# Kernel optimization log

Measured on AMD Instinct MI355X. Metric: run time of the kernel, lower is better.

## Reference

```python
import jax, jax.numpy as jnp
import numpy as np

N_LAYERS = 4   # last-4 BERT hidden layers summed by _Encoder
B, L, D = 4, 512, 768
LIN, ENT = 128, 10


def setup_inputs() -> dict:
    key = jax.random.key(0)
    k1, k2, k3, k4, k5 = jax.random.split(key, 5)
    return {
        "hidden_states": jax.random.normal(k1, (N_LAYERS, B, L, D), dtype=jnp.float32),
        "w_span": jax.random.normal(k2, (LIN, 2 * D), dtype=jnp.float32) * 0.02,
        "b_span": jax.random.normal(k3, (LIN,), dtype=jnp.float32) * 0.02,
        "w_cls": jax.random.normal(k4, (ENT, LIN), dtype=jnp.float32) * 0.02,
        "b_cls": jax.random.normal(k5, (ENT,), dtype=jnp.float32) * 0.02,
    }


def reference(hidden_states, w_span, b_span, w_cls, b_cls):
    # _Encoder: sum of last-4 hidden layers -> token embeddings (b, L, d)
    tok = jnp.sum(hidden_states, axis=0)
    d = tok.shape[-1]
    # Decompose span_linear weight into i-half and j-half so we never
    # materialize the (b, L, L, 2d) concat tensor. By linearity:
    #   Linear(cat(tok_i, tok_j)) = tok_i @ W1^T + tok_j @ W2^T + b
    w_i, w_j = w_span[:, :d], w_span[:, d:]
    proj_i = jnp.einsum("bld,od->blo", tok, w_i)   # (b, L, lin)
    proj_j = jnp.einsum("bld,od->blo", tok, w_j)   # (b, L, lin)
    span = proj_i[:, :, None, :] + proj_j[:, None, :, :] + b_span  # (b, L, L, lin)
    scores = jnp.einsum("bijo,co->bijc", span, w_cls) + b_cls      # (b, L, L, ent)
    return jnp.transpose(scores, (0, 3, 1, 2))  # (b, ent, L, L)
```

## Files before the change

### kernel.cpp

```cpp
#include <hip/hip_runtime.h>

#define NLAYER 4
#define BB 4
#define LL 512
#define DD 768
#define NLIN 128
#define NENT 10

#define OFF_CONST 15360
#define OFF_SI    15376
#define OFF_SJ    35856

__global__ void __launch_bounds__(256) fuse_weights(
    const float* __restrict__ w_span,
    const float* __restrict__ b_span,
    const float* __restrict__ w_cls,
    const float* __restrict__ b_cls,
    float* __restrict__ ws)
{
    int t = blockIdx.x * 256 + threadIdx.x;
    float* weff   = ws;
    float* constc = ws + OFF_CONST;

    if (t < 20 * DD) {
        int c2 = t / DD;
        int d  = t - c2 * DD;
        int ci   = (c2 < NENT) ? c2 : c2 - NENT;
        int half = (c2 < NENT) ? 0  : 1;
        const float* wc    = w_cls + ci * NLIN;
        const float* wsrow = w_span + half * DD + d;
        float acc = 0.f;
        #pragma unroll 8
        for (int o = 0; o < NLIN; ++o)
            acc += wc[o] * wsrow[(size_t)o * (2 * DD)];
        weff[c2 * DD + d] = acc;
    }
    if (t < NENT) {
        float cc = b_cls[t];
        const float* wc = w_cls + t * NLIN;
        for (int o = 0; o < NLIN; ++o) cc += b_span[o] * wc[o];
        constc[t] = cc;
    }
}

__global__ void __launch_bounds__(256) reduce_proj(
    const float* __restrict__ hs,
    const float* __restrict__ wsro,
    float* __restrict__ si,
    float* __restrict__ sj)
{
    __shared__ float wsh[20 * DD];

    {
        const float4* src = (const float4*)wsro;
        float4*       dst = (float4*)wsh;
        #pragma unroll
        for (int r = 0; r < 15; ++r)
            dst[r * 256 + threadIdx.x] = src[r * 256 + threadIdx.x];
    }
    __syncthreads();

    const int wave = (blockIdx.x * 256 + threadIdx.x) >> 6;
    const int lane = threadIdx.x & 63;
    const int b = wave >> 9;
    const int l = wave & 511;

    const size_t LAYER_STRIDE = (size_t)BB * LL * DD;
    const size_t base = (size_t)(b * LL + l) * DD;

    float acc[20];
    #pragma unroll
    for (int c = 0; c < 20; ++c) acc[c] = 0.f;

    #pragma unroll
    for (int k = 0; k < 3; ++k) {
        const int d0 = k * 256 + lane * 4;
        const float* hp = hs + base + d0;
        float4 t0 = *(const float4*)(hp);
        float4 t1 = *(const float4*)(hp + LAYER_STRIDE);
        float4 t2 = *(const float4*)(hp + 2 * LAYER_STRIDE);
        float4 t3 = *(const float4*)(hp + 3 * LAYER_STRIDE);
        float4 tv;
        tv.x = t0.x + t1.x + t2.x + t3.x;
        tv.y = t0.y + t1.y + t2.y + t3.y;
        tv.z = t0.z + t1.z + t2.z + t3.z;
        tv.w = t0.w + t1.w + t2.w + t3.w;
        const float* wbase = wsh + d0;
        #pragma unroll
        for (int c = 0; c < 20; ++c) {
            float4 w = *(const float4*)(wbase + c * DD);
            acc[c] += tv.x * w.x + tv.y * w.y + tv.z * w.z + tv.w * w.w;
        }
    }

    #pragma unroll
    for (int c = 0; c < 20; ++c) {
        float v = acc[c];
        v += __shfl_xor(v, 1,  64);
        v += __shfl_xor(v, 2,  64);
        v += __shfl_xor(v, 4,  64);
        v += __shfl_xor(v, 8,  64);
        v += __shfl_xor(v, 16, 64);
        v += __shfl_xor(v, 32, 64);
        acc[c] = v;
    }

    if (lane == 0) {
        const float* constc = wsro + OFF_CONST;
        const int rb = b * NENT;
        #pragma unroll
        for (int c = 0; c < NENT; ++c) {
            si[(rb + c) * LL + l] = acc[c] + constc[c];
            sj[(rb + c) * LL + l] = acc[10 + c];
        }
    }
}

__global__ void __launch_bounds__(256) fill_out(
    const float* __restrict__ si,
    const float* __restrict__ sj,
    float* __restrict__ out)
{
    const int idx4 = blockIdx.x * 256 + threadIdx.x;
    const int j4 = idx4 & 127;
    const int i  = (idx4 >> 7) & 511;
    const int bc = idx4 >> 16;
    const float  s  = si[bc * LL + i];
    const float4 v  = ((const float4*)(sj + bc * LL))[j4];
    float4 o;
    o.x = s + v.x; o.y = s + v.y; o.z = s + v.z; o.w = s + v.w;
    ((float4*)out)[idx4] = o;
}

extern "C" void kernel_launch(void* const* d_in, const int* in_sizes, int n_in,
                              void* d_out, int out_size, void* d_ws, size_t ws_size,
                              hipStream_t stream) {
    const float* hs     = (const float*)d_in[0];
    const float* w_span = (const float*)d_in[1];
    const float* b_span = (const float*)d_in[2];
    const float* w_cls  = (const float*)d_in[3];
    const float* b_cls  = (const float*)d_in[4];
    float* ws  = (float*)d_ws;
    float* out = (float*)d_out;
    float* si = ws + OFF_SI;
    float* sj = ws + OFF_SJ;

    fuse_weights<<<60, 256, 0, stream>>>(w_span, b_span, w_cls, b_cls, ws);
    reduce_proj<<<512, 256, 0, stream>>>(hs, ws, si, sj);
    fill_out<<<10240, 256, 0, stream>>>(si, sj, out);
}
```

Baseline: 105.1 us.

## Split weight fusion 4-way, prefetch hidden states before LDS staging, nontemporal output stores

fuse_weights now gives each output element to four threads, each covering a quarter of the 128-wide reduction, and combines them with shuffles, so the launch grows from 60 to 241 blocks. reduce_proj issues its hidden-state loads (nontemporal) into registers before writing the staged weights to shared memory, so global latency overlaps with the LDS fill and barrier. fill_out writes the large output with nontemporal stores to reduce cache pollution. The cost is higher register pressure in reduce_proj from holding 15 staged vectors plus 12 prefetched vectors.

Result: faster. 98.13 us (-6.7%).

```diff
diff --git a/kernel.cpp b/kernel.cpp
--- a/kernel.cpp
+++ b/kernel.cpp
@@ -11,6 +11,8 @@
 #define OFF_SI    15376
 #define OFF_SJ    35856
 
+typedef float vfloat4 __attribute__((ext_vector_type(4)));
+
 __global__ void __launch_bounds__(256) fuse_weights(
     const float* __restrict__ w_span,
     const float* __restrict__ b_span,
@@ -18,28 +20,36 @@
     const float* __restrict__ b_cls,
     float* __restrict__ ws)
 {
-    int t = blockIdx.x * 256 + threadIdx.x;
+    const int t   = blockIdx.x * 256 + threadIdx.x;
+    const int sub = t & 3;
+    const int idx = t >> 2;
     float* weff   = ws;
     float* constc = ws + OFF_CONST;
 
-    if (t < 20 * DD) {
-        int c2 = t / DD;
-        int d  = t - c2 * DD;
-        int ci   = (c2 < NENT) ? c2 : c2 - NENT;
-        int half = (c2 < NENT) ? 0  : 1;
-        const float* wc    = w_cls + ci * NLIN;
-        const float* wsrow = w_span + half * DD + d;
+    if (idx < 20 * DD) {
+        const int c2 = idx / DD;
+        const int d  = idx - c2 * DD;
+        const int ci   = (c2 < NENT) ? c2 : c2 - NENT;
+        const int half = (c2 < NENT) ? 0  : 1;
+        const float* wc    = w_cls + ci * NLIN + sub * 32;
+        const float* wsrow = w_span + (size_t)sub * 32 * (2 * DD) + half * DD + d;
         float acc = 0.f;
-        #pragma unroll 8
-        for (int o = 0; o < NLIN; ++o)
+        #pragma unroll
+        for (int o = 0; o < 32; ++o)
             acc += wc[o] * wsrow[(size_t)o * (2 * DD)];
-        weff[c2 * DD + d] = acc;
-    }
-    if (t < NENT) {
-        float cc = b_cls[t];
-        const float* wc = w_cls + t * NLIN;
-        for (int o = 0; o < NLIN; ++o) cc += b_span[o] * wc[o];
-        constc[t] = cc;
+        acc += __shfl_xor(acc, 1, 64);
+        acc += __shfl_xor(acc, 2, 64);
+        if (sub == 0) weff[c2 * DD + d] = acc;
+    } else if (idx < 20 * DD + NENT) {
+        const int c = idx - 20 * DD;
+        const float* wc = w_cls + c * NLIN + sub * 32;
+        const float* bs = b_span + sub * 32;
+        float cc = (sub == 0) ? b_cls[c] : 0.f;
+        #pragma unroll
+        for (int o = 0; o < 32; ++o) cc += bs[o] * wc[o];
+        cc += __shfl_xor(cc, 1, 64);
+        cc += __shfl_xor(cc, 2, 64);
+        if (sub == 0) constc[c] = cc;
     }
 }
 
@@ -51,22 +61,36 @@
 {
     __shared__ float wsh[20 * DD];
 
-    {
-        const float4* src = (const float4*)wsro;
-        float4*       dst = (float4*)wsh;
-        #pragma unroll
-        for (int r = 0; r < 15; ++r)
-            dst[r * 256 + threadIdx.x] = src[r * 256 + threadIdx.x];
-    }
-    __syncthreads();
-
-    const int wave = (blockIdx.x * 256 + threadIdx.x) >> 6;
-    const int lane = threadIdx.x & 63;
+    const int tid  = threadIdx.x;
+    const int wave = (blockIdx.x * 256 + tid) >> 6;
+    const int lane = tid & 63;
     const int b = wave >> 9;
     const int l = wave & 511;
 
     const size_t LAYER_STRIDE = (size_t)BB * LL * DD;
     const size_t base = (size_t)(b * LL + l) * DD;
+
+    const vfloat4* src = (const vfloat4*)wsro;
+    vfloat4 stg[15];
+    #pragma unroll
+    for (int r = 0; r < 15; ++r)
+        stg[r] = src[r * 256 + tid];
+
+    vfloat4 t0[3], t1[3], t2[3], t3[3];
+    #pragma unroll
+    for (int k = 0; k < 3; ++k) {
+        const float* hp = hs + base + k * 256 + lane * 4;
+        t0[k] = __builtin_nontemporal_load((const vfloat4*)(hp));
+        t1[k] = __builtin_nontemporal_load((const vfloat4*)(hp + LAYER_STRIDE));
+        t2[k] = __builtin_nontemporal_load((const vfloat4*)(hp + 2 * LAYER_STRIDE));
+        t3[k] = __builtin_nontemporal_load((const vfloat4*)(hp + 3 * LAYER_STRIDE));
+    }
+
+    vfloat4* dst = (vfloat4*)wsh;
+    #pragma unroll
+    for (int r = 0; r < 15; ++r)
+        dst[r * 256 + tid] = stg[r];
+    __syncthreads();
 
     float acc[20];
     #pragma unroll
@@ -74,21 +98,11 @@
 
     #pragma unroll
     for (int k = 0; k < 3; ++k) {
-        const int d0 = k * 256 + lane * 4;
-        const float* hp = hs + base + d0;
-        float4 t0 = *(const float4*)(hp);
-        float4 t1 = *(const float4*)(hp + LAYER_STRIDE);
-        float4 t2 = *(const float4*)(hp + 2 * LAYER_STRIDE);
-        float4 t3 = *(const float4*)(hp + 3 * LAYER_STRIDE);
-        float4 tv;
-        tv.x = t0.x + t1.x + t2.x + t3.x;
-        tv.y = t0.y + t1.y + t2.y + t3.y;
-        tv.z = t0.z + t1.z + t2.z + t3.z;
-        tv.w = t0.w + t1.w + t2.w + t3.w;
-        const float* wbase = wsh + d0;
+        vfloat4 tv = t0[k] + t1[k] + t2[k] + t3[k];
+        const float* wbase = wsh + k * 256 + lane * 4;
         #pragma unroll
         for (int c = 0; c < 20; ++c) {
-            float4 w = *(const float4*)(wbase + c * DD);
+            vfloat4 w = *(const vfloat4*)(wbase + c * DD);
             acc[c] += tv.x * w.x + tv.y * w.y + tv.z * w.z + tv.w * w.w;
         }
     }
@@ -125,11 +139,10 @@
     const int j4 = idx4 & 127;
     const int i  = (idx4 >> 7) & 511;
     const int bc = idx4 >> 16;
-    const float  s  = si[bc * LL + i];
-    const float4 v  = ((const float4*)(sj + bc * LL))[j4];
-    float4 o;
-    o.x = s + v.x; o.y = s + v.y; o.z = s + v.z; o.w = s + v.w;
-    ((float4*)out)[idx4] = o;
+    const float   s = si[bc * LL + i];
+    const vfloat4 v = ((const vfloat4*)(sj + bc * LL))[j4];
+    vfloat4 o = v + s;
+    __builtin_nontemporal_store(o, ((vfloat4*)out) + idx4);
 }
 
 extern "C" void kernel_launch(void* const* d_in, const int* in_sizes, int n_in,
@@ -145,7 +158,7 @@
     float* si = ws + OFF_SI;
     float* sj = ws + OFF_SJ;
 
-    fuse_weights<<<60, 256, 0, stream>>>(w_span, b_span, w_cls, b_cls, ws);
+    fuse_weights<<<241, 256, 0, stream>>>(w_span, b_span, w_cls, b_cls, ws);
     reduce_proj<<<512, 256, 0, stream>>>(hs, ws, si, sj);
     fill_out<<<10240, 256, 0, stream>>>(si, sj, out);
 }
```
